# Performance work log

Hardware: AMD Instinct MI355X
Metric: run time of the kernel (lower is better)

## Reference

```python
import jax, jax.numpy as jnp
import numpy as np

N_NODES = 50000
N_EDGES = 800000
IN_DIM = 128
OUT_DIM = 64


def setup_inputs() -> dict:
    key = jax.random.key(0)
    k1, k2, k3, k4 = jax.random.split(key, 4)
    x = jax.random.normal(k1, (N_NODES, IN_DIM), dtype=jnp.float32)
    edge_index = jax.random.randint(k2, (2, N_EDGES), 0, N_NODES, dtype=jnp.int64)
    # learned params: W: Linear(in_dim, out_dim, bias=False); att: Linear(2*out_dim, 1, bias=False)
    W = jax.random.normal(k3, (IN_DIM, OUT_DIM), dtype=jnp.float32) * 0.05
    att = jax.random.normal(k4, (2 * OUT_DIM, 1), dtype=jnp.float32) * 0.05
    return {"x": x, "edge_index": edge_index, "W": W, "att": att}


def reference(x, edge_index, W, att):
    n = x.shape[0]
    h = x @ W  # [N, D]
    src, dst = edge_index[0], edge_index[1]
    # per-edge attention logit: leaky_relu(att^T [h_src ; h_dst])
    e = jnp.concatenate([h[src], h[dst]], axis=-1) @ att  # [E, 1]
    e = jax.nn.leaky_relu(e[:, 0], negative_slope=0.2)  # [E]
    # segment softmax over edges grouped by destination node
    m = jax.ops.segment_max(e, dst, num_segments=n)  # [N]
    ex = jnp.exp(e - m[dst])  # [E]
    denom = jax.ops.segment_sum(ex, dst, num_segments=n)  # [N]
    alpha = ex / denom[dst]  # [E]
    # weighted scatter-add aggregation
    agg = jax.ops.segment_sum(alpha[:, None] * h[src], dst, num_segments=n)  # [N, D]
    return jax.nn.elu(agg)
```

## Files before the change

kernel.cpp:

```cpp
#include <hip/hip_runtime.h>
#include <hip/hip_bf16.h>
#include <hip/hip_fp16.h>
#include <math.h>

#define N_NODES 50000
#define N_EDGES 800000
#define IN_DIM 128
#define OUT_DIM 64

typedef __attribute__((ext_vector_type(8))) short bf16x8;
typedef __attribute__((ext_vector_type(4))) float f32x4;

static __device__ __forceinline__ uint f2bf(float f) {
  uint u = __float_as_uint(f);
  return (u + 0x7fffu + ((u >> 16) & 1u)) >> 16;
}

#define N4 (N_NODES / 4)
#define SCAN_NB ((N4 + 255) / 256)
#define GEMM_NB ((N_NODES + 63) / 64)
#define K2_T (N_EDGES / 2)
#define K4_T (N_EDGES / 8)

__global__ __launch_bounds__(256) void k0_prep(const float* __restrict__ W,
                                               int* __restrict__ deg,
                                               ushort* __restrict__ WTfrag) {
  int t = blockIdx.x * 256 + threadIdx.x;
  if (t < N4) ((int4*)deg)[t] = make_int4(0, 0, 0, 0);
  if (t < IN_DIM * OUT_DIM) {
    int j = t & 7, l = (t >> 3) & 63, ks = (t >> 9) & 3, nt = (t >> 11) & 3;
    int c = nt * 16 + (l & 15);
    int k = ks * 32 + ((l >> 4) << 3) + j;
    WTfrag[t] = (ushort)f2bf(W[(size_t)k * OUT_DIM + c]);
  }
}

__global__ __launch_bounds__(256, 4) void k1_mfma(
    const float* __restrict__ x, const ushort* __restrict__ WTfrag,
    const float* __restrict__ att,
    __half* __restrict__ h, float* __restrict__ a1, float* __restrict__ a2) {
  __shared__ __align__(16) ushort Ah[64 * 128];

  int tid = threadIdx.x;
  int row0 = blockIdx.x * 64;

#pragma unroll
  for (int it = 0; it < 8; ++it) {
    int i4 = it * 256 + tid;
    int row = i4 >> 5;
    int kq = i4 & 31;
    int grow = row0 + row;
    if (grow > N_NODES - 1) grow = N_NODES - 1;
    float4 v = ((const float4*)x)[(size_t)grow * 32 + kq];
    uint2 hv = make_uint2(f2bf(v.x) | (f2bf(v.y) << 16),
                          f2bf(v.z) | (f2bf(v.w) << 16));
    int idx = (row * 128 + kq * 4) ^ ((row & 7) << 3);
    *(uint2*)&Ah[idx] = hv;
  }
  __syncthreads();

  int w = tid >> 6, l = tid & 63;
  int ml = l & 15, kg = l >> 4;
  const bf16x8* __restrict__ Bf = (const bf16x8*)WTfrag;

  f32x4 acc[4];
#pragma unroll
  for (int nt = 0; nt < 4; ++nt) acc[nt] = (f32x4){0.f, 0.f, 0.f, 0.f};

#pragma unroll
  for (int ks = 0; ks < 4; ++ks) {
    int arow = w * 16 + ml;
    int aidx = (arow * 128 + ks * 32 + kg * 8) ^ ((arow & 7) << 3);
    bf16x8 a_h = *(const bf16x8*)&Ah[aidx];
#pragma unroll
    for (int nt = 0; nt < 4; ++nt) {
      bf16x8 b = Bf[(nt * 4 + ks) * 64 + l];
      acc[nt] = __builtin_amdgcn_mfma_f32_16x16x32_bf16(a_h, b, acc[nt], 0, 0, 0);
    }
  }

  float t1[4], t2[4];
#pragma unroll
  for (int nt = 0; nt < 4; ++nt) {
    t1[nt] = att[nt * 16 + ml];
    t2[nt] = att[OUT_DIM + nt * 16 + ml];
  }
#pragma unroll
  for (int r = 0; r < 4; ++r) {
    int drow = kg * 4 + r;
    int grow = row0 + w * 16 + drow;
    bool ok = grow < N_NODES;
    float p1 = 0.f, p2 = 0.f;
#pragma unroll
    for (int nt = 0; nt < 4; ++nt) {
      float d = acc[nt][r];
      if (ok) h[(size_t)grow * OUT_DIM + nt * 16 + ml] = __float2half(d);
      p1 = fmaf(d, t1[nt], p1);
      p2 = fmaf(d, t2[nt], p2);
    }
#pragma unroll
    for (int o = 1; o <= 8; o <<= 1) {
      p1 += __shfl_xor(p1, o, 64);
      p2 += __shfl_xor(p2, o, 64);
    }
    if (ml == 0 && ok) { a1[grow] = p1; a2[grow] = p2; }
  }
}

__global__ __launch_bounds__(256) void k2_rank(const int* __restrict__ dstp,
                                               int* __restrict__ deg,
                                               int* __restrict__ rank) {
  int t = blockIdx.x * 256 + threadIdx.x;
  if (t >= K2_T) return;
  int2 d = ((const int2*)dstp)[t];
  int2 r;
  r.x = atomicAdd(&deg[d.x], 1);
  r.y = atomicAdd(&deg[d.y], 1);
  ((int2*)rank)[t] = r;
}

__global__ __launch_bounds__(256) void k3_scan(const int* __restrict__ deg,
                                               int* __restrict__ off,
                                               int* __restrict__ bsum) {
  __shared__ int sw[4];
  int tid = threadIdx.x, lane = tid & 63, wid = tid >> 6;
  int i4 = blockIdx.x * 256 + tid;
  int4 v = make_int4(0, 0, 0, 0);
  if (i4 < N4) v = ((const int4*)deg)[i4];
  int local = v.x + v.y + v.z + v.w;
  int incl = local;
#pragma unroll
  for (int o = 1; o < 64; o <<= 1) {
    int t = __shfl_up(incl, o, 64);
    if (lane >= o) incl += t;
  }
  if (lane == 63) sw[wid] = incl;
  __syncthreads();
  if (tid == 0) {
    int c = 0;
#pragma unroll
    for (int ww = 0; ww < 4; ++ww) { int t = sw[ww]; sw[ww] = c; c += t; }
    bsum[blockIdx.x] = c;
  }
  __syncthreads();
  int excl = incl - local + sw[wid];
  int4 o;
  o.x = excl; o.y = o.x + v.x; o.z = o.y + v.y; o.w = o.z + v.z;
  if (i4 < N4) ((int4*)off)[i4] = o;
}

__device__ __forceinline__ void scan_bsum_to_lds(const int* __restrict__ bsum,
                                                 int* sBX, int tid) {
  if (tid < 64) {
    int v = (tid < SCAN_NB) ? bsum[tid] : 0;
    int incl = v;
#pragma unroll
    for (int o = 1; o < 64; o <<= 1) {
      int t = __shfl_up(incl, o, 64);
      if (tid >= o) incl += t;
    }
    sBX[tid] = incl - v;
  }
  __syncthreads();
}

__global__ __launch_bounds__(256) void k4_scatter(
    const int* __restrict__ src, const int* __restrict__ dstp,
    const int* __restrict__ rank, const int* __restrict__ bsum,
    const float* __restrict__ a1, const float* __restrict__ a2,
    const int* __restrict__ off, int2* __restrict__ sedge) {
  __shared__ int sBX[64];
  int tid = threadIdx.x;
  scan_bsum_to_lds(bsum, sBX, tid);

  int t = blockIdx.x * 256 + tid;
  if (t >= K4_T) return;
  int4 s0 = ((const int4*)src)[t * 2],  s1 = ((const int4*)src)[t * 2 + 1];
  int4 d0 = ((const int4*)dstp)[t * 2], d1 = ((const int4*)dstp)[t * 2 + 1];
  int4 r0 = ((const int4*)rank)[t * 2], r1 = ((const int4*)rank)[t * 2 + 1];
  int S[8] = {s0.x, s0.y, s0.z, s0.w, s1.x, s1.y, s1.z, s1.w};
  int D[8] = {d0.x, d0.y, d0.z, d0.w, d1.x, d1.y, d1.z, d1.w};
  int R[8] = {r0.x, r0.y, r0.z, r0.w, r1.x, r1.y, r1.z, r1.w};
  float A[8], B[8];
  int O[8];
#pragma unroll
  for (int q = 0; q < 8; ++q) {
    A[q] = a1[S[q]];
    B[q] = a2[D[q]];
    O[q] = off[D[q]];
  }
#pragma unroll
  for (int q = 0; q < 8; ++q) {
    float e = A[q] + B[q];
    e = e > 0.f ? e : 0.2f * e;
    int p = O[q] + sBX[D[q] >> 10] + R[q];
    sedge[p] = make_int2(S[q], __float_as_int(__expf(e)));
  }
}

__global__ __launch_bounds__(256) void k5_agg(
    const int* __restrict__ off, const int* __restrict__ bsum,
    const int2* __restrict__ sedge,
    const __half* __restrict__ h, float* __restrict__ out) {
  __shared__ int sBX[64];
  int tid = threadIdx.x;
  scan_bsum_to_lds(bsum, sBX, tid);

  int g = tid >> 3, gl = tid & 7;
  int n = blockIdx.x * 32 + g;
  if (n >= N_NODES) return;
  int b = off[n] + sBX[n >> 10];
  int e = (n + 1 < N_NODES) ? (off[n + 1] + sBX[(n + 1) >> 10]) : N_EDGES;

  float sum = 0.f;
  float a0 = 0.f, a1_ = 0.f, a2_ = 0.f, a3 = 0.f;
  float a4 = 0.f, a5 = 0.f, a6 = 0.f, a7 = 0.f;
  const __half* __restrict__ hb = h;

#define K5_ACC(rr, ww)                                                        \
  {                                                                           \
    float2 f;                                                                 \
    f = __half22float2(__builtin_bit_cast(__half2, rr.x));                    \
    a0 = fmaf(ww, f.x, a0); a1_ = fmaf(ww, f.y, a1_);                         \
    f = __half22float2(__builtin_bit_cast(__half2, rr.y));                    \
    a2_ = fmaf(ww, f.x, a2_); a3 = fmaf(ww, f.y, a3);                         \
    f = __half22float2(__builtin_bit_cast(__half2, rr.z));                    \
    a4 = fmaf(ww, f.x, a4); a5 = fmaf(ww, f.y, a5);                           \
    f = __half22float2(__builtin_bit_cast(__half2, rr.w));                    \
    a6 = fmaf(ww, f.x, a6); a7 = fmaf(ww, f.y, a7);                           \
  }

  int j = b;
  for (; j + 7 < e; j += 8) {
    int2 s0 = sedge[j + 0], s1 = sedge[j + 1], s2 = sedge[j + 2], s3 = sedge[j + 3];
    int2 s4 = sedge[j + 4], s5 = sedge[j + 5], s6 = sedge[j + 6], s7 = sedge[j + 7];
    uint4 r0 = ((const uint4*)(hb + (size_t)s0.x * OUT_DIM))[gl];
    uint4 r1 = ((const uint4*)(hb + (size_t)s1.x * OUT_DIM))[gl];
    uint4 r2 = ((const uint4*)(hb + (size_t)s2.x * OUT_DIM))[gl];
    uint4 r3 = ((const uint4*)(hb + (size_t)s3.x * OUT_DIM))[gl];
    uint4 r4 = ((const uint4*)(hb + (size_t)s4.x * OUT_DIM))[gl];
    uint4 r5 = ((const uint4*)(hb + (size_t)s5.x * OUT_DIM))[gl];
    uint4 r6 = ((const uint4*)(hb + (size_t)s6.x * OUT_DIM))[gl];
    uint4 r7 = ((const uint4*)(hb + (size_t)s7.x * OUT_DIM))[gl];
    float w0 = __int_as_float(s0.y), w1 = __int_as_float(s1.y);
    float w2 = __int_as_float(s2.y), w3 = __int_as_float(s3.y);
    float w4 = __int_as_float(s4.y), w5 = __int_as_float(s5.y);
    float w6 = __int_as_float(s6.y), w7 = __int_as_float(s7.y);
    sum += ((w0 + w1) + (w2 + w3)) + ((w4 + w5) + (w6 + w7));
    K5_ACC(r0, w0); K5_ACC(r1, w1); K5_ACC(r2, w2); K5_ACC(r3, w3);
    K5_ACC(r4, w4); K5_ACC(r5, w5); K5_ACC(r6, w6); K5_ACC(r7, w7);
  }
  for (; j + 3 < e; j += 4) {
    int2 s0 = sedge[j + 0], s1 = sedge[j + 1], s2 = sedge[j + 2], s3 = sedge[j + 3];
    uint4 r0 = ((const uint4*)(hb + (size_t)s0.x * OUT_DIM))[gl];
    uint4 r1 = ((const uint4*)(hb + (size_t)s1.x * OUT_DIM))[gl];
    uint4 r2 = ((const uint4*)(hb + (size_t)s2.x * OUT_DIM))[gl];
    uint4 r3 = ((const uint4*)(hb + (size_t)s3.x * OUT_DIM))[gl];
    float w0 = __int_as_float(s0.y), w1 = __int_as_float(s1.y);
    float w2 = __int_as_float(s2.y), w3 = __int_as_float(s3.y);
    sum += (w0 + w1) + (w2 + w3);
    K5_ACC(r0, w0); K5_ACC(r1, w1); K5_ACC(r2, w2); K5_ACC(r3, w3);
  }
  for (; j < e; ++j) {
    int2 s0 = sedge[j];
    uint4 r0 = ((const uint4*)(hb + (size_t)s0.x * OUT_DIM))[gl];
    float w0 = __int_as_float(s0.y);
    sum += w0;
    K5_ACC(r0, w0);
  }

  float inv = (e > b) ? 1.f / sum : 0.f;
  a0 *= inv; a1_ *= inv; a2_ *= inv; a3 *= inv;
  a4 *= inv; a5 *= inv; a6 *= inv; a7 *= inv;
  float4 o0, o1;
  o0.x = a0 > 0.f ? a0 : (__expf(a0) - 1.f);
  o0.y = a1_ > 0.f ? a1_ : (__expf(a1_) - 1.f);
  o0.z = a2_ > 0.f ? a2_ : (__expf(a2_) - 1.f);
  o0.w = a3 > 0.f ? a3 : (__expf(a3) - 1.f);
  o1.x = a4 > 0.f ? a4 : (__expf(a4) - 1.f);
  o1.y = a5 > 0.f ? a5 : (__expf(a5) - 1.f);
  o1.z = a6 > 0.f ? a6 : (__expf(a6) - 1.f);
  o1.w = a7 > 0.f ? a7 : (__expf(a7) - 1.f);
  float4* ob = (float4*)(out + (size_t)n * OUT_DIM);
  ob[gl * 2] = o0;
  ob[gl * 2 + 1] = o1;
}

extern "C" void kernel_launch(void* const* d_in, const int* in_sizes, int n_in,
                              void* d_out, int out_size, void* d_ws, size_t ws_size,
                              hipStream_t stream) {
  const float* x   = (const float*)d_in[0];
  const int*   ei  = (const int*)d_in[1];
  const float* W   = (const float*)d_in[2];
  const float* att = (const float*)d_in[3];
  float* out = (float*)d_out;

  char* p = (char*)d_ws;
  __half* h  = (__half*)p;  p += (size_t)N_NODES * OUT_DIM * sizeof(__half);
  float* a1  = (float*)p;   p += (size_t)N_NODES * sizeof(float);
  float* a2  = (float*)p;   p += (size_t)N_NODES * sizeof(float);
  int*   deg = (int*)p;     p += (size_t)N_NODES * sizeof(int);
  int*   off = (int*)p;     p += (size_t)(N_NODES + 4) * sizeof(int);
  int*   rank = (int*)p;    p += (size_t)N_EDGES * sizeof(int);
  int2*  sedge = (int2*)p;  p += (size_t)N_EDGES * sizeof(int2);
  int*   bsum = (int*)p;    p += 64 * sizeof(int);
  ushort* WTfrag = (ushort*)p; p += (size_t)OUT_DIM * IN_DIM * sizeof(ushort);

  const int* src  = ei;
  const int* dstp = ei + N_EDGES;

  k0_prep<<<SCAN_NB, 256, 0, stream>>>(W, deg, WTfrag);
  k2_rank<<<(K2_T + 255) / 256, 256, 0, stream>>>(dstp, deg, rank);
  k1_mfma<<<GEMM_NB, 256, 0, stream>>>(x, WTfrag, att, h, a1, a2);
  k3_scan<<<SCAN_NB, 256, 0, stream>>>(deg, off, bsum);
  k4_scatter<<<(K4_T + 255) / 256, 256, 0, stream>>>(src, dstp, rank, bsum, a1, a2, off, sedge);
  k5_agg<<<(N_NODES + 31) / 32, 256, 0, stream>>>(off, bsum, sedge, h, out);
}
```

Measured before the change: 99.34 us.

## Fuse all stages into one persistent cooperative kernel with grid syncs

Merges the six separate launches (prep, rank, GEMM, scan, scatter, aggregate) into one cooperative kernel of 512 blocks that loops over work and separates phases with grid.sync(). Odd blocks run the rank atomics before their GEMM tiles and even blocks after, so the two independent stages overlap. The aim is to remove per-launch overhead and idle gaps between kernels. In exchange, each grid barrier has a cost, occupancy is capped by the persistent grid, and the aggregation loop loses its 8-wide unroll.

```diff
diff --git a/kernel.cpp b/kernel.cpp
--- a/kernel.cpp
+++ b/kernel.cpp
@@ -1,7 +1,10 @@
 #include <hip/hip_runtime.h>
+#include <hip/hip_cooperative_groups.h>
 #include <hip/hip_bf16.h>
 #include <hip/hip_fp16.h>
 #include <math.h>
+
+namespace cg = cooperative_groups;
 
 #define N_NODES 50000
 #define N_EDGES 800000
@@ -19,138 +22,139 @@
 #define N4 (N_NODES / 4)
 #define SCAN_NB ((N4 + 255) / 256)
 #define GEMM_NB ((N_NODES + 63) / 64)
-#define K2_T (N_EDGES / 2)
+#define E2 (N_EDGES / 2)
 #define K4_T (N_EDGES / 8)
-
-__global__ __launch_bounds__(256) void k0_prep(const float* __restrict__ W,
-                                               int* __restrict__ deg,
-                                               ushort* __restrict__ WTfrag) {
-  int t = blockIdx.x * 256 + threadIdx.x;
-  if (t < N4) ((int4*)deg)[t] = make_int4(0, 0, 0, 0);
-  if (t < IN_DIM * OUT_DIM) {
+#define K5_U ((N_NODES + 31) / 32)
+
+#define GRID_NB 512
+#define NTHREADS (GRID_NB * 256)
+
+__global__ __launch_bounds__(256, 4) void mono(
+    const float* __restrict__ x, const int* __restrict__ src,
+    const int* __restrict__ dstp, const float* __restrict__ W,
+    const float* __restrict__ att, __half* __restrict__ h,
+    float* __restrict__ a1, float* __restrict__ a2, int* __restrict__ deg,
+    int* __restrict__ off, int* __restrict__ rank, int2* __restrict__ sedge,
+    int* __restrict__ bsum, ushort* __restrict__ WTfrag,
+    float* __restrict__ out) {
+  cg::grid_group grid = cg::this_grid();
+  __shared__ __align__(16) ushort Ah[64 * 128];
+  __shared__ int sw[4];
+  __shared__ int sBX[64];
+
+  int tid = threadIdx.x, bid = blockIdx.x;
+  int gt = bid * 256 + tid;
+
+  for (int t = gt; t < N4; t += NTHREADS) ((int4*)deg)[t] = make_int4(0, 0, 0, 0);
+  for (int t = gt; t < IN_DIM * OUT_DIM; t += NTHREADS) {
     int j = t & 7, l = (t >> 3) & 63, ks = (t >> 9) & 3, nt = (t >> 11) & 3;
     int c = nt * 16 + (l & 15);
     int k = ks * 32 + ((l >> 4) << 3) + j;
     WTfrag[t] = (ushort)f2bf(W[(size_t)k * OUT_DIM + c]);
   }
-}
-
-__global__ __launch_bounds__(256, 4) void k1_mfma(
-    const float* __restrict__ x, const ushort* __restrict__ WTfrag,
-    const float* __restrict__ att,
-    __half* __restrict__ h, float* __restrict__ a1, float* __restrict__ a2) {
-  __shared__ __align__(16) ushort Ah[64 * 128];
-
-  int tid = threadIdx.x;
-  int row0 = blockIdx.x * 64;
-
-#pragma unroll
-  for (int it = 0; it < 8; ++it) {
-    int i4 = it * 256 + tid;
-    int row = i4 >> 5;
-    int kq = i4 & 31;
-    int grow = row0 + row;
-    if (grow > N_NODES - 1) grow = N_NODES - 1;
-    float4 v = ((const float4*)x)[(size_t)grow * 32 + kq];
-    uint2 hv = make_uint2(f2bf(v.x) | (f2bf(v.y) << 16),
-                          f2bf(v.z) | (f2bf(v.w) << 16));
-    int idx = (row * 128 + kq * 4) ^ ((row & 7) << 3);
-    *(uint2*)&Ah[idx] = hv;
-  }
-  __syncthreads();
+  grid.sync();
 
   int w = tid >> 6, l = tid & 63;
   int ml = l & 15, kg = l >> 4;
-  const bf16x8* __restrict__ Bf = (const bf16x8*)WTfrag;
-
-  f32x4 acc[4];
-#pragma unroll
-  for (int nt = 0; nt < 4; ++nt) acc[nt] = (f32x4){0.f, 0.f, 0.f, 0.f};
-
-#pragma unroll
-  for (int ks = 0; ks < 4; ++ks) {
-    int arow = w * 16 + ml;
-    int aidx = (arow * 128 + ks * 32 + kg * 8) ^ ((arow & 7) << 3);
-    bf16x8 a_h = *(const bf16x8*)&Ah[aidx];
-#pragma unroll
-    for (int nt = 0; nt < 4; ++nt) {
-      bf16x8 b = Bf[(nt * 4 + ks) * 64 + l];
-      acc[nt] = __builtin_amdgcn_mfma_f32_16x16x32_bf16(a_h, b, acc[nt], 0, 0, 0);
-    }
-  }
-
-  float t1[4], t2[4];
-#pragma unroll
-  for (int nt = 0; nt < 4; ++nt) {
-    t1[nt] = att[nt * 16 + ml];
-    t2[nt] = att[OUT_DIM + nt * 16 + ml];
-  }
-#pragma unroll
-  for (int r = 0; r < 4; ++r) {
-    int drow = kg * 4 + r;
-    int grow = row0 + w * 16 + drow;
-    bool ok = grow < N_NODES;
-    float p1 = 0.f, p2 = 0.f;
-#pragma unroll
-    for (int nt = 0; nt < 4; ++nt) {
-      float d = acc[nt][r];
-      if (ok) h[(size_t)grow * OUT_DIM + nt * 16 + ml] = __float2half(d);
-      p1 = fmaf(d, t1[nt], p1);
-      p2 = fmaf(d, t2[nt], p2);
-    }
-#pragma unroll
-    for (int o = 1; o <= 8; o <<= 1) {
-      p1 += __shfl_xor(p1, o, 64);
-      p2 += __shfl_xor(p2, o, 64);
-    }
-    if (ml == 0 && ok) { a1[grow] = p1; a2[grow] = p2; }
-  }
-}
-
-__global__ __launch_bounds__(256) void k2_rank(const int* __restrict__ dstp,
-                                               int* __restrict__ deg,
-                                               int* __restrict__ rank) {
-  int t = blockIdx.x * 256 + threadIdx.x;
-  if (t >= K2_T) return;
-  int2 d = ((const int2*)dstp)[t];
-  int2 r;
-  r.x = atomicAdd(&deg[d.x], 1);
-  r.y = atomicAdd(&deg[d.y], 1);
-  ((int2*)rank)[t] = r;
-}
-
-__global__ __launch_bounds__(256) void k3_scan(const int* __restrict__ deg,
-                                               int* __restrict__ off,
-                                               int* __restrict__ bsum) {
-  __shared__ int sw[4];
-  int tid = threadIdx.x, lane = tid & 63, wid = tid >> 6;
-  int i4 = blockIdx.x * 256 + tid;
-  int4 v = make_int4(0, 0, 0, 0);
-  if (i4 < N4) v = ((const int4*)deg)[i4];
-  int local = v.x + v.y + v.z + v.w;
-  int incl = local;
-#pragma unroll
-  for (int o = 1; o < 64; o <<= 1) {
-    int t = __shfl_up(incl, o, 64);
-    if (lane >= o) incl += t;
-  }
-  if (lane == 63) sw[wid] = incl;
-  __syncthreads();
-  if (tid == 0) {
-    int c = 0;
-#pragma unroll
-    for (int ww = 0; ww < 4; ++ww) { int t = sw[ww]; sw[ww] = c; c += t; }
-    bsum[blockIdx.x] = c;
-  }
-  __syncthreads();
-  int excl = incl - local + sw[wid];
-  int4 o;
-  o.x = excl; o.y = o.x + v.x; o.z = o.y + v.y; o.w = o.z + v.z;
-  if (i4 < N4) ((int4*)off)[i4] = o;
-}
-
-__device__ __forceinline__ void scan_bsum_to_lds(const int* __restrict__ bsum,
-                                                 int* sBX, int tid) {
+
+  auto do_gemm = [&]() {
+    const bf16x8* __restrict__ Bf = (const bf16x8*)WTfrag;
+    for (int tile = bid; tile < GEMM_NB; tile += GRID_NB) {
+      __syncthreads();
+      int row0 = tile * 64;
+#pragma unroll
+      for (int it = 0; it < 8; ++it) {
+        int i4 = it * 256 + tid;
+        int row = i4 >> 5;
+        int kq = i4 & 31;
+        int grow = row0 + row;
+        if (grow > N_NODES - 1) grow = N_NODES - 1;
+        float4 v = ((const float4*)x)[(size_t)grow * 32 + kq];
+        uint2 hv = make_uint2(f2bf(v.x) | (f2bf(v.y) << 16),
+                              f2bf(v.z) | (f2bf(v.w) << 16));
+        int idx = (row * 128 + kq * 4) ^ ((row & 7) << 3);
+        *(uint2*)&Ah[idx] = hv;
+      }
+      __syncthreads();
+
+      f32x4 acc[4];
+#pragma unroll
+      for (int nt = 0; nt < 4; ++nt) acc[nt] = (f32x4){0.f, 0.f, 0.f, 0.f};
+#pragma unroll
+      for (int ks = 0; ks < 4; ++ks) {
+        int arow = w * 16 + ml;
+        int aidx = (arow * 128 + ks * 32 + kg * 8) ^ ((arow & 7) << 3);
+        bf16x8 a_h = *(const bf16x8*)&Ah[aidx];
+#pragma unroll
+        for (int nt = 0; nt < 4; ++nt) {
+          bf16x8 b = Bf[(nt * 4 + ks) * 64 + l];
+          acc[nt] = __builtin_amdgcn_mfma_f32_16x16x32_bf16(a_h, b, acc[nt], 0, 0, 0);
+        }
+      }
+#pragma unroll
+      for (int r = 0; r < 4; ++r) {
+        int grow = row0 + w * 16 + kg * 4 + r;
+        bool ok = grow < N_NODES;
+        float p1 = 0.f, p2 = 0.f;
+#pragma unroll
+        for (int nt = 0; nt < 4; ++nt) {
+          float d = acc[nt][r];
+          if (ok) h[(size_t)grow * OUT_DIM + nt * 16 + ml] = __float2half(d);
+          p1 = fmaf(d, att[nt * 16 + ml], p1);
+          p2 = fmaf(d, att[OUT_DIM + nt * 16 + ml], p2);
+        }
+#pragma unroll
+        for (int o = 1; o <= 8; o <<= 1) {
+          p1 += __shfl_xor(p1, o, 64);
+          p2 += __shfl_xor(p2, o, 64);
+        }
+        if (ml == 0 && ok) { a1[grow] = p1; a2[grow] = p2; }
+      }
+    }
+  };
+
+  auto do_rank = [&]() {
+    for (int t = gt; t < E2; t += NTHREADS) {
+      int2 d = ((const int2*)dstp)[t];
+      int2 r;
+      r.x = atomicAdd(&deg[d.x], 1);
+      r.y = atomicAdd(&deg[d.y], 1);
+      ((int2*)rank)[t] = r;
+    }
+  };
+
+  if (bid & 1) { do_rank(); do_gemm(); }
+  else         { do_gemm(); do_rank(); }
+  grid.sync();
+
+  if (bid < SCAN_NB) {
+    int lane = tid & 63, wid = tid >> 6;
+    int i4 = bid * 256 + tid;
+    int4 v = make_int4(0, 0, 0, 0);
+    if (i4 < N4) v = ((const int4*)deg)[i4];
+    int local = v.x + v.y + v.z + v.w;
+    int incl = local;
+#pragma unroll
+    for (int o = 1; o < 64; o <<= 1) {
+      int t = __shfl_up(incl, o, 64);
+      if (lane >= o) incl += t;
+    }
+    if (lane == 63) sw[wid] = incl;
+    __syncthreads();
+    if (tid == 0) {
+      int c = 0;
+#pragma unroll
+      for (int ww = 0; ww < 4; ++ww) { int t = sw[ww]; sw[ww] = c; c += t; }
+      bsum[bid] = c;
+    }
+    __syncthreads();
+    int excl = incl - local + sw[wid];
+    int4 o;
+    o.x = excl; o.y = o.x + v.x; o.z = o.y + v.y; o.w = o.z + v.z;
+    if (i4 < N4) ((int4*)off)[i4] = o;
+  }
+  grid.sync();
+
   if (tid < 64) {
     int v = (tid < SCAN_NB) ? bsum[tid] : 0;
     int incl = v;
@@ -162,60 +166,44 @@
     sBX[tid] = incl - v;
   }
   __syncthreads();
-}
-
-__global__ __launch_bounds__(256) void k4_scatter(
-    const int* __restrict__ src, const int* __restrict__ dstp,
-    const int* __restrict__ rank, const int* __restrict__ bsum,
-    const float* __restrict__ a1, const float* __restrict__ a2,
-    const int* __restrict__ off, int2* __restrict__ sedge) {
-  __shared__ int sBX[64];
-  int tid = threadIdx.x;
-  scan_bsum_to_lds(bsum, sBX, tid);
-
-  int t = blockIdx.x * 256 + tid;
-  if (t >= K4_T) return;
-  int4 s0 = ((const int4*)src)[t * 2],  s1 = ((const int4*)src)[t * 2 + 1];
-  int4 d0 = ((const int4*)dstp)[t * 2], d1 = ((const int4*)dstp)[t * 2 + 1];
-  int4 r0 = ((const int4*)rank)[t * 2], r1 = ((const int4*)rank)[t * 2 + 1];
-  int S[8] = {s0.x, s0.y, s0.z, s0.w, s1.x, s1.y, s1.z, s1.w};
-  int D[8] = {d0.x, d0.y, d0.z, d0.w, d1.x, d1.y, d1.z, d1.w};
-  int R[8] = {r0.x, r0.y, r0.z, r0.w, r1.x, r1.y, r1.z, r1.w};
-  float A[8], B[8];
-  int O[8];
-#pragma unroll
-  for (int q = 0; q < 8; ++q) {
-    A[q] = a1[S[q]];
-    B[q] = a2[D[q]];
-    O[q] = off[D[q]];
-  }
-#pragma unroll
-  for (int q = 0; q < 8; ++q) {
-    float e = A[q] + B[q];
-    e = e > 0.f ? e : 0.2f * e;
-    int p = O[q] + sBX[D[q] >> 10] + R[q];
-    sedge[p] = make_int2(S[q], __float_as_int(__expf(e)));
-  }
-}
-
-__global__ __launch_bounds__(256) void k5_agg(
-    const int* __restrict__ off, const int* __restrict__ bsum,
-    const int2* __restrict__ sedge,
-    const __half* __restrict__ h, float* __restrict__ out) {
-  __shared__ int sBX[64];
-  int tid = threadIdx.x;
-  scan_bsum_to_lds(bsum, sBX, tid);
+
+  if (gt < K4_T) {
+    int t = gt;
+    int4 s0 = ((const int4*)src)[t * 2],  s1 = ((const int4*)src)[t * 2 + 1];
+    int4 d0 = ((const int4*)dstp)[t * 2], d1 = ((const int4*)dstp)[t * 2 + 1];
+    int4 r0 = ((const int4*)rank)[t * 2], r1 = ((const int4*)rank)[t * 2 + 1];
+    int S[8] = {s0.x, s0.y, s0.z, s0.w, s1.x, s1.y, s1.z, s1.w};
+    int D[8] = {d0.x, d0.y, d0.z, d0.w, d1.x, d1.y, d1.z, d1.w};
+    int R[8] = {r0.x, r0.y, r0.z, r0.w, r1.x, r1.y, r1.z, r1.w};
+    float A[8], B[8];
+    int O[8];
+#pragma unroll
+    for (int q = 0; q < 8; ++q) {
+      A[q] = a1[S[q]];
+      B[q] = a2[D[q]];
+      O[q] = off[D[q]];
+    }
+#pragma unroll
+    for (int q = 0; q < 8; ++q) {
+      float e = A[q] + B[q];
+      e = e > 0.f ? e : 0.2f * e;
+      int p = O[q] + sBX[D[q] >> 10] + R[q];
+      sedge[p] = make_int2(S[q], __float_as_int(__expf(e)));
+    }
+  }
+  grid.sync();
 
   int g = tid >> 3, gl = tid & 7;
-  int n = blockIdx.x * 32 + g;
-  if (n >= N_NODES) return;
-  int b = off[n] + sBX[n >> 10];
-  int e = (n + 1 < N_NODES) ? (off[n + 1] + sBX[(n + 1) >> 10]) : N_EDGES;
-
-  float sum = 0.f;
-  float a0 = 0.f, a1_ = 0.f, a2_ = 0.f, a3 = 0.f;
-  float a4 = 0.f, a5 = 0.f, a6 = 0.f, a7 = 0.f;
-  const __half* __restrict__ hb = h;
+  for (int u = bid; u < K5_U; u += GRID_NB) {
+    int n = u * 32 + g;
+    if (n >= N_NODES) continue;
+    int b = off[n] + sBX[n >> 10];
+    int e = (n + 1 < N_NODES) ? (off[n + 1] + sBX[(n + 1) >> 10]) : N_EDGES;
+
+    float sum = 0.f;
+    float a0 = 0.f, a1_ = 0.f, a2_ = 0.f, a3 = 0.f;
+    float a4 = 0.f, a5 = 0.f, a6 = 0.f, a7 = 0.f;
+    const __half* __restrict__ hb = h;
 
 #define K5_ACC(rr, ww)                                                        \
   {                                                                           \
@@ -230,60 +218,42 @@
     a6 = fmaf(ww, f.x, a6); a7 = fmaf(ww, f.y, a7);                           \
   }
 
-  int j = b;
-  for (; j + 7 < e; j += 8) {
-    int2 s0 = sedge[j + 0], s1 = sedge[j + 1], s2 = sedge[j + 2], s3 = sedge[j + 3];
-    int2 s4 = sedge[j + 4], s5 = sedge[j + 5], s6 = sedge[j + 6], s7 = sedge[j + 7];
-    uint4 r0 = ((const uint4*)(hb + (size_t)s0.x * OUT_DIM))[gl];
-    uint4 r1 = ((const uint4*)(hb + (size_t)s1.x * OUT_DIM))[gl];
-    uint4 r2 = ((const uint4*)(hb + (size_t)s2.x * OUT_DIM))[gl];
-    uint4 r3 = ((const uint4*)(hb + (size_t)s3.x * OUT_DIM))[gl];
-    uint4 r4 = ((const uint4*)(hb + (size_t)s4.x * OUT_DIM))[gl];
-    uint4 r5 = ((const uint4*)(hb + (size_t)s5.x * OUT_DIM))[gl];
-    uint4 r6 = ((const uint4*)(hb + (size_t)s6.x * OUT_DIM))[gl];
-    uint4 r7 = ((const uint4*)(hb + (size_t)s7.x * OUT_DIM))[gl];
-    float w0 = __int_as_float(s0.y), w1 = __int_as_float(s1.y);
-    float w2 = __int_as_float(s2.y), w3 = __int_as_float(s3.y);
-    float w4 = __int_as_float(s4.y), w5 = __int_as_float(s5.y);
-    float w6 = __int_as_float(s6.y), w7 = __int_as_float(s7.y);
-    sum += ((w0 + w1) + (w2 + w3)) + ((w4 + w5) + (w6 + w7));
-    K5_ACC(r0, w0); K5_ACC(r1, w1); K5_ACC(r2, w2); K5_ACC(r3, w3);
-    K5_ACC(r4, w4); K5_ACC(r5, w5); K5_ACC(r6, w6); K5_ACC(r7, w7);
-  }
-  for (; j + 3 < e; j += 4) {
-    int2 s0 = sedge[j + 0], s1 = sedge[j + 1], s2 = sedge[j + 2], s3 = sedge[j + 3];
-    uint4 r0 = ((const uint4*)(hb + (size_t)s0.x * OUT_DIM))[gl];
-    uint4 r1 = ((const uint4*)(hb + (size_t)s1.x * OUT_DIM))[gl];
-    uint4 r2 = ((const uint4*)(hb + (size_t)s2.x * OUT_DIM))[gl];
-    uint4 r3 = ((const uint4*)(hb + (size_t)s3.x * OUT_DIM))[gl];
-    float w0 = __int_as_float(s0.y), w1 = __int_as_float(s1.y);
-    float w2 = __int_as_float(s2.y), w3 = __int_as_float(s3.y);
-    sum += (w0 + w1) + (w2 + w3);
-    K5_ACC(r0, w0); K5_ACC(r1, w1); K5_ACC(r2, w2); K5_ACC(r3, w3);
-  }
-  for (; j < e; ++j) {
-    int2 s0 = sedge[j];
-    uint4 r0 = ((const uint4*)(hb + (size_t)s0.x * OUT_DIM))[gl];
-    float w0 = __int_as_float(s0.y);
-    sum += w0;
-    K5_ACC(r0, w0);
-  }
-
-  float inv = (e > b) ? 1.f / sum : 0.f;
-  a0 *= inv; a1_ *= inv; a2_ *= inv; a3 *= inv;
-  a4 *= inv; a5 *= inv; a6 *= inv; a7 *= inv;
-  float4 o0, o1;
-  o0.x = a0 > 0.f ? a0 : (__expf(a0) - 1.f);
-  o0.y = a1_ > 0.f ? a1_ : (__expf(a1_) - 1.f);
-  o0.z = a2_ > 0.f ? a2_ : (__expf(a2_) - 1.f);
-  o0.w = a3 > 0.f ? a3 : (__expf(a3) - 1.f);
-  o1.x = a4 > 0.f ? a4 : (__expf(a4) - 1.f);
-  o1.y = a5 > 0.f ? a5 : (__expf(a5) - 1.f);
-  o1.z = a6 > 0.f ? a6 : (__expf(a6) - 1.f);
-  o1.w = a7 > 0.f ? a7 : (__expf(a7) - 1.f);
-  float4* ob = (float4*)(out + (size_t)n * OUT_DIM);
-  ob[gl * 2] = o0;
-  ob[gl * 2 + 1] = o1;
+    int j = b;
+    for (; j + 3 < e; j += 4) {
+      int2 s0 = sedge[j + 0], s1 = sedge[j + 1], s2 = sedge[j + 2], s3 = sedge[j + 3];
+      uint4 r0 = ((const uint4*)(hb + (size_t)s0.x * OUT_DIM))[gl];
+      uint4 r1 = ((const uint4*)(hb + (size_t)s1.x * OUT_DIM))[gl];
+      uint4 r2 = ((const uint4*)(hb + (size_t)s2.x * OUT_DIM))[gl];
+      uint4 r3 = ((const uint4*)(hb + (size_t)s3.x * OUT_DIM))[gl];
+      float w0 = __int_as_float(s0.y), w1 = __int_as_float(s1.y);
+      float w2 = __int_as_float(s2.y), w3 = __int_as_float(s3.y);
+      sum += (w0 + w1) + (w2 + w3);
+      K5_ACC(r0, w0); K5_ACC(r1, w1); K5_ACC(r2, w2); K5_ACC(r3, w3);
+    }
+    for (; j < e; ++j) {
+      int2 s0 = sedge[j];
+      uint4 r0 = ((const uint4*)(hb + (size_t)s0.x * OUT_DIM))[gl];
+      float w0 = __int_as_float(s0.y);
+      sum += w0;
+      K5_ACC(r0, w0);
+    }
+
+    float inv = (e > b) ? 1.f / sum : 0.f;
+    a0 *= inv; a1_ *= inv; a2_ *= inv; a3 *= inv;
+    a4 *= inv; a5 *= inv; a6 *= inv; a7 *= inv;
+    float4 o0, o1;
+    o0.x = a0 > 0.f ? a0 : (__expf(a0) - 1.f);
+    o0.y = a1_ > 0.f ? a1_ : (__expf(a1_) - 1.f);
+    o0.z = a2_ > 0.f ? a2_ : (__expf(a2_) - 1.f);
+    o0.w = a3 > 0.f ? a3 : (__expf(a3) - 1.f);
+    o1.x = a4 > 0.f ? a4 : (__expf(a4) - 1.f);
+    o1.y = a5 > 0.f ? a5 : (__expf(a5) - 1.f);
+    o1.z = a6 > 0.f ? a6 : (__expf(a6) - 1.f);
+    o1.w = a7 > 0.f ? a7 : (__expf(a7) - 1.f);
+    float4* ob = (float4*)(out + (size_t)n * OUT_DIM);
+    ob[gl * 2] = o0;
+    ob[gl * 2 + 1] = o1;
+  }
 }
 
 extern "C" void kernel_launch(void* const* d_in, const int* in_sizes, int n_in,
@@ -309,10 +279,10 @@
   const int* src  = ei;
   const int* dstp = ei + N_EDGES;
 
-  k0_prep<<<SCAN_NB, 256, 0, stream>>>(W, deg, WTfrag);
-  k2_rank<<<(K2_T + 255) / 256, 256, 0, stream>>>(dstp, deg, rank);
-  k1_mfma<<<GEMM_NB, 256, 0, stream>>>(x, WTfrag, att, h, a1, a2);
-  k3_scan<<<SCAN_NB, 256, 0, stream>>>(deg, off, bsum);
-  k4_scatter<<<(K4_T + 255) / 256, 256, 0, stream>>>(src, dstp, rank, bsum, a1, a2, off, sedge);
-  k5_agg<<<(N_NODES + 31) / 32, 256, 0, stream>>>(off, bsum, sedge, h, out);
+  void* args[] = {(void*)&x,   (void*)&src, (void*)&dstp, (void*)&W,
+                  (void*)&att, (void*)&h,   (void*)&a1,   (void*)&a2,
+                  (void*)&deg, (void*)&off, (void*)&rank, (void*)&sedge,
+                  (void*)&bsum, (void*)&WTfrag, (void*)&out};
+  hipLaunchCooperativeKernel((const void*)mono, dim3(GRID_NB), dim3(256),
+                             args, 0, stream);
 }
```

Result: slower. 321.5 us (+223.7%).
